# Optimization experiments

Hardware: AMD Instinct MI355X
Metric: run time of the kernel (lower is better)

Reference implementation:

```python
import jax, jax.numpy as jnp
import numpy as np

H = 64  # LSTM hidden size

def _lstm_layer(x, Wih, Whh, bih, bhh):
    # x: [B,T,I]; PyTorch gate order (i, f, g, o); zero initial state
    B, T, _ = x.shape
    pre = jnp.einsum('bti,gi->btg', x, Wih) + bih + bhh  # [B,T,4H]
    def step(carry, p):
        h, c = carry
        g = p + h @ Whh.T
        i, f, gg, o = jnp.split(g, 4, axis=-1)
        c = jax.nn.sigmoid(f) * c + jax.nn.sigmoid(i) * jnp.tanh(gg)
        h = jax.nn.sigmoid(o) * jnp.tanh(c)
        return (h, c), h
    h0 = jnp.zeros((B, H), x.dtype)
    c0 = jnp.zeros((B, H), x.dtype)
    _, hs = jax.lax.scan(step, (h0, c0), jnp.swapaxes(pre, 0, 1))
    return jnp.swapaxes(hs, 0, 1)  # [B,T,H]

def _lstm_params(key, in_dim):
    s = 1.0 / np.sqrt(H)
    k1, k2, k3, k4 = jax.random.split(key, 4)
    return (jax.random.uniform(k1, (4 * H, in_dim), jnp.float32, -s, s),
            jax.random.uniform(k2, (4 * H, H), jnp.float32, -s, s),
            jax.random.uniform(k3, (4 * H,), jnp.float32, -s, s),
            jax.random.uniform(k4, (4 * H,), jnp.float32, -s, s))

def setup_inputs() -> dict:
    key = jax.random.key(0)
    ks = jax.random.split(key, 9)
    B, T = 1024, 1024
    x = jax.random.normal(ks[0], (B, T, 3), jnp.float32)
    e1 = _lstm_params(ks[1], 3)
    e2 = _lstm_params(ks[2], H)
    d1 = _lstm_params(ks[3], 5)
    d2 = _lstm_params(ks[4], H)
    s = 1.0 / np.sqrt(H)
    enc_fc_W = jax.random.uniform(ks[5], (5, H), jnp.float32, -s, s)
    enc_fc_b = jax.random.uniform(ks[6], (5,), jnp.float32, -s, s)
    dec_fc_W = jax.random.uniform(ks[7], (3, H), jnp.float32, -s, s)
    dec_fc_b = jax.random.uniform(ks[8], (3,), jnp.float32, -s, s)
    return {
        'x': x,
        'e1_Wih': e1[0], 'e1_Whh': e1[1], 'e1_bih': e1[2], 'e1_bhh': e1[3],
        'e2_Wih': e2[0], 'e2_Whh': e2[1], 'e2_bih': e2[2], 'e2_bhh': e2[3],
        'enc_fc_W': enc_fc_W, 'enc_fc_b': enc_fc_b,
        'd1_Wih': d1[0], 'd1_Whh': d1[1], 'd1_bih': d1[2], 'd1_bhh': d1[3],
        'd2_Wih': d2[0], 'd2_Whh': d2[1], 'd2_bih': d2[2], 'd2_bhh': d2[3],
        'dec_fc_W': dec_fc_W, 'dec_fc_b': dec_fc_b,
    }

def reference(x,
              e1_Wih, e1_Whh, e1_bih, e1_bhh,
              e2_Wih, e2_Whh, e2_bih, e2_bhh,
              enc_fc_W, enc_fc_b,
              d1_Wih, d1_Whh, d1_bih, d1_bhh,
              d2_Wih, d2_Whh, d2_bih, d2_bhh,
              dec_fc_W, dec_fc_b):
    h = _lstm_layer(x, e1_Wih, e1_Whh, e1_bih, e1_bhh)
    h = _lstm_layer(h, e2_Wih, e2_Whh, e2_bih, e2_bhh)
    u = h[:, -1, :] @ enc_fc_W.T + enc_fc_b        # [B,5]
    u = u[:, None, :]                               # [B,1,5]
    d = _lstm_layer(u, d1_Wih, d1_Whh, d1_bih, d1_bhh)
    d = _lstm_layer(d, d2_Wih, d2_Whh, d2_bih, d2_bhh)
    tau = d[:, -1, :] @ dec_fc_W.T + dec_fc_b       # [B,3]
    return (u, tau)
```

## Files before the change

### kernel.cpp

```cpp
#include <hip/hip_runtime.h>
#include <stdint.h>

typedef _Float16 f16x8 __attribute__((ext_vector_type(8)));
typedef float f32x4 __attribute__((ext_vector_type(4)));

__device__ __forceinline__ float sigf(float x) {
    return __builtin_amdgcn_rcpf(1.0f + __expf(-x));
}
__device__ __forceinline__ float tanhf_fast(float x) {
    return 1.0f - 2.0f * __builtin_amdgcn_rcpf(1.0f + __expf(2.0f * x));
}
__device__ __forceinline__ uint32_t pk2f(float a, float b) {
    uint16_t ua = __builtin_bit_cast(uint16_t, (_Float16)a);
    uint16_t ub = __builtin_bit_cast(uint16_t, (_Float16)b);
    return (uint32_t)ua | ((uint32_t)ub << 16);
}

__global__ __launch_bounds__(512, 1)
void lstm_mfma16(const float* __restrict__ x,
                 const float* __restrict__ W1i, const float* __restrict__ W1h,
                 const float* __restrict__ b1i, const float* __restrict__ b1h,
                 const float* __restrict__ W2i, const float* __restrict__ W2h,
                 const float* __restrict__ b2i, const float* __restrict__ b2h,
                 const float* __restrict__ eW,  const float* __restrict__ eb,
                 const float* __restrict__ D1i, const float* __restrict__ D1bi,
                 const float* __restrict__ D1bh,
                 const float* __restrict__ D2i, const float* __restrict__ D2bi,
                 const float* __restrict__ D2bh,
                 const float* __restrict__ dW,  const float* __restrict__ db,
                 float* __restrict__ out)
{
    __shared__ __align__(16) _Float16 h1b[2][16][72];
    __shared__ __align__(16) _Float16 h2b[2][16][72];
    __shared__ __align__(16) _Float16 xs[2][16][16][8];
    __shared__ float uW[8][8];
    __shared__ float tlA[8][64];
    __shared__ float tlB[8][64];

    const int tid = threadIdx.x, blk = blockIdx.x;
    const int wid = tid >> 6, lane = tid & 63;
    const int rl = lane & 15, hi = lane >> 4;
    const bool isL1 = (wid < 4);
    const int w = isL1 ? wid : wid - 4;

    {
        uint32_t* z1 = (uint32_t*)&h1b[0][0][0];
        for (int i = tid; i < 1152; i += 512) z1[i] = 0u;
        uint32_t* z2 = (uint32_t*)&h2b[0][0][0];
        for (int i = tid; i < 1152; i += 512) z2[i] = 0u;
        uint32_t* z3 = (uint32_t*)&xs[0][0][0][0];
        for (int i = tid; i < 2048; i += 512) z3[i] = 0u;
    }

    f16x8 afr[4][4];
    #pragma unroll
    for (int g = 0; g < 4; ++g) {
        const int grow = g * 64 + w * 16 + rl;
        if (isL1) {
            #pragma unroll
            for (int s = 0; s < 2; ++s) {
                f16x8 v;
                #pragma unroll
                for (int i = 0; i < 8; ++i)
                    v[i] = (_Float16)W1h[grow * 64 + s * 32 + hi * 8 + i];
                afr[g][s] = v;
            }
            {
                f16x8 v;
                #pragma unroll
                for (int i = 0; i < 8; ++i) {
                    int kk = hi * 8 + i;
                    v[i] = (kk < 3) ? (_Float16)W1i[grow * 3 + kk] : (_Float16)0.0f;
                }
                afr[g][2] = v;
            }
            {
                f16x8 v;
                #pragma unroll
                for (int i = 0; i < 8; ++i) v[i] = (_Float16)0.0f;
                afr[g][3] = v;
            }
        } else {
            #pragma unroll
            for (int s = 0; s < 2; ++s) {
                f16x8 v;
                #pragma unroll
                for (int i = 0; i < 8; ++i)
                    v[i] = (_Float16)W2i[grow * 64 + s * 32 + hi * 8 + i];
                afr[g][s] = v;
            }
            #pragma unroll
            for (int s = 0; s < 2; ++s) {
                f16x8 v;
                #pragma unroll
                for (int i = 0; i < 8; ++i)
                    v[i] = (_Float16)W2h[grow * 64 + s * 32 + hi * 8 + i];
                afr[g][2 + s] = v;
            }
        }
    }

    f32x4 bias[4];
    #pragma unroll
    for (int g = 0; g < 4; ++g) {
        #pragma unroll
        for (int r = 0; r < 4; ++r) {
            int grow = g * 64 + w * 16 + hi * 4 + r;
            bias[g][r] = isL1 ? (b1i[grow] + b1h[grow]) : (b2i[grow] + b2h[grow]);
        }
    }

    float cst[4] = {0.0f, 0.0f, 0.0f, 0.0f};

    const int tt = tid >> 4, sA = tid & 15;
    const float* xsrc = x + (size_t)(blk * 16 + sA) * 3072;
    float xr0 = 0.f, xr1 = 0.f, xr2 = 0.f;

    __syncthreads();

    if (tid < 256) {
        const float* xp = xsrc + (size_t)tt * 3;
        uint2 pk;
        pk.x = pk2f(xp[0], xp[1]);
        pk.y = pk2f(xp[2], 0.0f);
        *(uint2*)&xs[0][tt][sA][0] = pk;
    }
    __syncthreads();

    #pragma unroll 1
    for (int t = 0; t <= 1024; ++t) {
        const int p = t & 1;
        const int cb = (t >> 4) & 1;

        if ((t & 15) == 0 && (t + 16) < 1024 && tid < 256) {
            const float* xp = xsrc + (size_t)(t + 16 + tt) * 3;
            xr0 = xp[0]; xr1 = xp[1]; xr2 = xp[2];
        }

        if (isL1 && t < 1024) {
            f32x4 a0 = bias[0], a1 = bias[1], a2 = bias[2], a3 = bias[3];
            #pragma unroll
            for (int s = 0; s < 2; ++s) {
                f16x8 bf = *(const f16x8*)&h1b[p][rl][s * 32 + hi * 8];
                a0 = __builtin_amdgcn_mfma_f32_16x16x32_f16(afr[0][s], bf, a0, 0, 0, 0);
                a1 = __builtin_amdgcn_mfma_f32_16x16x32_f16(afr[1][s], bf, a1, 0, 0, 0);
                a2 = __builtin_amdgcn_mfma_f32_16x16x32_f16(afr[2][s], bf, a2, 0, 0, 0);
                a3 = __builtin_amdgcn_mfma_f32_16x16x32_f16(afr[3][s], bf, a3, 0, 0, 0);
            }
            {
                f16x8 bf = {};
                if (hi == 0) bf = *(const f16x8*)&xs[cb][t & 15][rl][0];
                a0 = __builtin_amdgcn_mfma_f32_16x16x32_f16(afr[0][2], bf, a0, 0, 0, 0);
                a1 = __builtin_amdgcn_mfma_f32_16x16x32_f16(afr[1][2], bf, a1, 0, 0, 0);
                a2 = __builtin_amdgcn_mfma_f32_16x16x32_f16(afr[2][2], bf, a2, 0, 0, 0);
                a3 = __builtin_amdgcn_mfma_f32_16x16x32_f16(afr[3][2], bf, a3, 0, 0, 0);
            }
            uint16_t hu[4];
            #pragma unroll
            for (int r = 0; r < 4; ++r) {
                float pi = a0[r], pf = a1[r], pgg = a2[r], po = a3[r];
                cst[r] = sigf(pf) * cst[r] + sigf(pi) * tanhf_fast(pgg);
                float hn = sigf(po) * tanhf_fast(cst[r]);
                hu[r] = __builtin_bit_cast(uint16_t, (_Float16)hn);
            }
            uint2 pk;
            pk.x = (uint32_t)hu[0] | ((uint32_t)hu[1] << 16);
            pk.y = (uint32_t)hu[2] | ((uint32_t)hu[3] << 16);
            *(uint2*)&h1b[p ^ 1][rl][w * 16 + hi * 4] = pk;
        } else if (!isL1 && t >= 1) {
            f32x4 a0 = bias[0], a1 = bias[1], a2 = bias[2], a3 = bias[3];
            #pragma unroll
            for (int s = 0; s < 2; ++s) {
                f16x8 bf = *(const f16x8*)&h1b[p][rl][s * 32 + hi * 8];
                a0 = __builtin_amdgcn_mfma_f32_16x16x32_f16(afr[0][s], bf, a0, 0, 0, 0);
                a1 = __builtin_amdgcn_mfma_f32_16x16x32_f16(afr[1][s], bf, a1, 0, 0, 0);
                a2 = __builtin_amdgcn_mfma_f32_16x16x32_f16(afr[2][s], bf, a2, 0, 0, 0);
                a3 = __builtin_amdgcn_mfma_f32_16x16x32_f16(afr[3][s], bf, a3, 0, 0, 0);
            }
            #pragma unroll
            for (int s = 0; s < 2; ++s) {
                f16x8 bf = *(const f16x8*)&h2b[p][rl][s * 32 + hi * 8];
                a0 = __builtin_amdgcn_mfma_f32_16x16x32_f16(afr[0][2 + s], bf, a0, 0, 0, 0);
                a1 = __builtin_amdgcn_mfma_f32_16x16x32_f16(afr[1][2 + s], bf, a1, 0, 0, 0);
                a2 = __builtin_amdgcn_mfma_f32_16x16x32_f16(afr[2][2 + s], bf, a2, 0, 0, 0);
                a3 = __builtin_amdgcn_mfma_f32_16x16x32_f16(afr[3][2 + s], bf, a3, 0, 0, 0);
            }
            uint16_t hu[4];
            #pragma unroll
            for (int r = 0; r < 4; ++r) {
                float pi = a0[r], pf = a1[r], pgg = a2[r], po = a3[r];
                cst[r] = sigf(pf) * cst[r] + sigf(pi) * tanhf_fast(pgg);
                float hn = sigf(po) * tanhf_fast(cst[r]);
                hu[r] = __builtin_bit_cast(uint16_t, (_Float16)hn);
            }
            uint2 pk;
            pk.x = (uint32_t)hu[0] | ((uint32_t)hu[1] << 16);
            pk.y = (uint32_t)hu[2] | ((uint32_t)hu[3] << 16);
            *(uint2*)&h2b[p ^ 1][rl][w * 16 + hi * 4] = pk;
        }

        if ((t & 15) == 15 && (t + 1) < 1024 && tid < 256) {
            uint2 pk;
            pk.x = pk2f(xr0, xr1);
            pk.y = pk2f(xr2, 0.0f);
            *(uint2*)&xs[cb ^ 1][tt][sA][0] = pk;
        }
        __syncthreads();
    }

    #pragma unroll 1
    for (int ss = 0; ss < 2; ++ss) {
        const int s = wid * 2 + ss;
        const int S = blk * 16 + s;

        if (lane < 5) {
            float acc = eb[lane];
            for (int k = 0; k < 64; ++k)
                acc += eW[lane * 64 + k] * (float)h2b[1][s][k];
            uW[wid][lane] = acc;
            out[S * 5 + lane] = acc;
        }
        __syncthreads();

        {
            float u0 = uW[wid][0], u1 = uW[wid][1], u2 = uW[wid][2],
                  u3 = uW[wid][3], u4 = uW[wid][4];
            int ri = lane, rg = 128 + lane, ro = 192 + lane;
            float pi = D1bi[ri] + D1bh[ri];
            float pg = D1bi[rg] + D1bh[rg];
            float po = D1bi[ro] + D1bh[ro];
            pi += D1i[ri*5+0]*u0 + D1i[ri*5+1]*u1 + D1i[ri*5+2]*u2 + D1i[ri*5+3]*u3 + D1i[ri*5+4]*u4;
            pg += D1i[rg*5+0]*u0 + D1i[rg*5+1]*u1 + D1i[rg*5+2]*u2 + D1i[rg*5+3]*u3 + D1i[rg*5+4]*u4;
            po += D1i[ro*5+0]*u0 + D1i[ro*5+1]*u1 + D1i[ro*5+2]*u2 + D1i[ro*5+3]*u3 + D1i[ro*5+4]*u4;
            float cd = sigf(pi) * tanhf_fast(pg);
            float hd = sigf(po) * tanhf_fast(cd);
            tlA[wid][lane] = hd;
        }
        __syncthreads();

        {
            int ri = lane, rg = 128 + lane, ro = 192 + lane;
            float pi = D2bi[ri] + D2bh[ri];
            float pg = D2bi[rg] + D2bh[rg];
            float po = D2bi[ro] + D2bh[ro];
            for (int k = 0; k < 64; ++k) {
                float hk = tlA[wid][k];
                pi += D2i[ri * 64 + k] * hk;
                pg += D2i[rg * 64 + k] * hk;
                po += D2i[ro * 64 + k] * hk;
            }
            float cd = sigf(pi) * tanhf_fast(pg);
            float hd = sigf(po) * tanhf_fast(cd);
            tlB[wid][lane] = hd;
        }
        __syncthreads();

        if (lane < 3) {
            float acc = db[lane];
            for (int k = 0; k < 64; ++k) acc += dW[lane * 64 + k] * tlB[wid][k];
            out[5120 + S * 3 + lane] = acc;
        }
        __syncthreads();
    }
}

extern "C" void kernel_launch(void* const* d_in, const int* in_sizes, int n_in,
                              void* d_out, int out_size, void* d_ws, size_t ws_size,
                              hipStream_t stream) {
    (void)in_sizes; (void)n_in; (void)out_size; (void)d_ws; (void)ws_size;
    const float* x    = (const float*)d_in[0];
    const float* W1i  = (const float*)d_in[1];
    const float* W1h  = (const float*)d_in[2];
    const float* b1i  = (const float*)d_in[3];
    const float* b1h  = (const float*)d_in[4];
    const float* W2i  = (const float*)d_in[5];
    const float* W2h  = (const float*)d_in[6];
    const float* b2i  = (const float*)d_in[7];
    const float* b2h  = (const float*)d_in[8];
    const float* eW   = (const float*)d_in[9];
    const float* eb   = (const float*)d_in[10];
    const float* D1i  = (const float*)d_in[11];
    const float* D1bi = (const float*)d_in[13];
    const float* D1bh = (const float*)d_in[14];
    const float* D2i  = (const float*)d_in[15];
    const float* D2bi = (const float*)d_in[17];
    const float* D2bh = (const float*)d_in[18];
    const float* dW   = (const float*)d_in[19];
    const float* db   = (const float*)d_in[20];

    hipLaunchKernelGGL(lstm_mfma16, dim3(64), dim3(512), 0, stream,
                       x, W1i, W1h, b1i, b1h, W2i, W2h, b2i, b2h, eW, eb,
                       D1i, D1bi, D1bh, D2i, D2bi, D2bh, dW, db,
                       (float*)d_out);
}
```

Baseline: 984.0 us.

## Halve sequences per block to 8, doubling grid, and prescale gate weights by log2e

```diff
diff --git a/kernel.cpp b/kernel.cpp
--- a/kernel.cpp
+++ b/kernel.cpp
@@ -1,9 +1,18 @@
 #include <hip/hip_runtime.h>
 #include <stdint.h>
+#include <math.h>
 
 typedef _Float16 f16x8 __attribute__((ext_vector_type(8)));
 typedef float f32x4 __attribute__((ext_vector_type(4)));
 
+#define LOG2E 1.44269504088896340736f
+
+__device__ __forceinline__ float sigp(float p) {
+    return __builtin_amdgcn_rcpf(1.0f + exp2f(-p));
+}
+__device__ __forceinline__ float tanhg(float p) {
+    return 1.0f - 2.0f * __builtin_amdgcn_rcpf(1.0f + exp2f(p));
+}
 __device__ __forceinline__ float sigf(float x) {
     return __builtin_amdgcn_rcpf(1.0f + __expf(-x));
 }
@@ -17,18 +26,18 @@
 }
 
 __global__ __launch_bounds__(512, 1)
-void lstm_mfma16(const float* __restrict__ x,
-                 const float* __restrict__ W1i, const float* __restrict__ W1h,
-                 const float* __restrict__ b1i, const float* __restrict__ b1h,
-                 const float* __restrict__ W2i, const float* __restrict__ W2h,
-                 const float* __restrict__ b2i, const float* __restrict__ b2h,
-                 const float* __restrict__ eW,  const float* __restrict__ eb,
-                 const float* __restrict__ D1i, const float* __restrict__ D1bi,
-                 const float* __restrict__ D1bh,
-                 const float* __restrict__ D2i, const float* __restrict__ D2bi,
-                 const float* __restrict__ D2bh,
-                 const float* __restrict__ dW,  const float* __restrict__ db,
-                 float* __restrict__ out)
+void lstm_mfma8(const float* __restrict__ x,
+                const float* __restrict__ W1i, const float* __restrict__ W1h,
+                const float* __restrict__ b1i, const float* __restrict__ b1h,
+                const float* __restrict__ W2i, const float* __restrict__ W2h,
+                const float* __restrict__ b2i, const float* __restrict__ b2h,
+                const float* __restrict__ eW,  const float* __restrict__ eb,
+                const float* __restrict__ D1i, const float* __restrict__ D1bi,
+                const float* __restrict__ D1bh,
+                const float* __restrict__ D2i, const float* __restrict__ D2bi,
+                const float* __restrict__ D2bh,
+                const float* __restrict__ dW,  const float* __restrict__ db,
+                float* __restrict__ out)
 {
     __shared__ __align__(16) _Float16 h1b[2][16][72];
     __shared__ __align__(16) _Float16 h2b[2][16][72];
@@ -52,17 +61,20 @@
         for (int i = tid; i < 2048; i += 512) z3[i] = 0u;
     }
 
+    const float gsc[4] = {LOG2E, LOG2E, 2.0f * LOG2E, LOG2E};
+
     f16x8 afr[4][4];
     #pragma unroll
     for (int g = 0; g < 4; ++g) {
         const int grow = g * 64 + w * 16 + rl;
+        const float sc = gsc[g];
         if (isL1) {
             #pragma unroll
             for (int s = 0; s < 2; ++s) {
                 f16x8 v;
                 #pragma unroll
                 for (int i = 0; i < 8; ++i)
-                    v[i] = (_Float16)W1h[grow * 64 + s * 32 + hi * 8 + i];
+                    v[i] = (_Float16)(sc * W1h[grow * 64 + s * 32 + hi * 8 + i]);
                 afr[g][s] = v;
             }
             {
@@ -70,7 +82,7 @@
                 #pragma unroll
                 for (int i = 0; i < 8; ++i) {
                     int kk = hi * 8 + i;
-                    v[i] = (kk < 3) ? (_Float16)W1i[grow * 3 + kk] : (_Float16)0.0f;
+                    v[i] = (kk < 3) ? (_Float16)(sc * W1i[grow * 3 + kk]) : (_Float16)0.0f;
                 }
                 afr[g][2] = v;
             }
@@ -86,7 +98,7 @@
                 f16x8 v;
                 #pragma unroll
                 for (int i = 0; i < 8; ++i)
-                    v[i] = (_Float16)W2i[grow * 64 + s * 32 + hi * 8 + i];
+                    v[i] = (_Float16)(sc * W2i[grow * 64 + s * 32 + hi * 8 + i]);
                 afr[g][s] = v;
             }
             #pragma unroll
@@ -94,7 +106,7 @@
                 f16x8 v;
                 #pragma unroll
                 for (int i = 0; i < 8; ++i)
-                    v[i] = (_Float16)W2h[grow * 64 + s * 32 + hi * 8 + i];
+                    v[i] = (_Float16)(sc * W2h[grow * 64 + s * 32 + hi * 8 + i]);
                 afr[g][2 + s] = v;
             }
         }
@@ -106,19 +118,20 @@
         #pragma unroll
         for (int r = 0; r < 4; ++r) {
             int grow = g * 64 + w * 16 + hi * 4 + r;
-            bias[g][r] = isL1 ? (b1i[grow] + b1h[grow]) : (b2i[grow] + b2h[grow]);
+            bias[g][r] = gsc[g] * (isL1 ? (b1i[grow] + b1h[grow])
+                                        : (b2i[grow] + b2h[grow]));
         }
     }
 
     float cst[4] = {0.0f, 0.0f, 0.0f, 0.0f};
 
-    const int tt = tid >> 4, sA = tid & 15;
-    const float* xsrc = x + (size_t)(blk * 16 + sA) * 3072;
+    const int tt = tid >> 3, sA = tid & 7;
+    const float* xsrc = x + (size_t)(blk * 8 + sA) * 3072;
     float xr0 = 0.f, xr1 = 0.f, xr2 = 0.f;
 
     __syncthreads();
 
-    if (tid < 256) {
+    if (tid < 128) {
         const float* xp = xsrc + (size_t)tt * 3;
         uint2 pk;
         pk.x = pk2f(xp[0], xp[1]);
@@ -132,7 +145,7 @@
         const int p = t & 1;
         const int cb = (t >> 4) & 1;
 
-        if ((t & 15) == 0 && (t + 16) < 1024 && tid < 256) {
+        if ((t & 15) == 0 && (t + 16) < 1024 && tid < 128) {
             const float* xp = xsrc + (size_t)(t + 16 + tt) * 3;
             xr0 = xp[0]; xr1 = xp[1]; xr2 = xp[2];
         }
@@ -155,18 +168,20 @@
                 a2 = __builtin_amdgcn_mfma_f32_16x16x32_f16(afr[2][2], bf, a2, 0, 0, 0);
                 a3 = __builtin_amdgcn_mfma_f32_16x16x32_f16(afr[3][2], bf, a3, 0, 0, 0);
             }
-            uint16_t hu[4];
-            #pragma unroll
-            for (int r = 0; r < 4; ++r) {
-                float pi = a0[r], pf = a1[r], pgg = a2[r], po = a3[r];
-                cst[r] = sigf(pf) * cst[r] + sigf(pi) * tanhf_fast(pgg);
-                float hn = sigf(po) * tanhf_fast(cst[r]);
-                hu[r] = __builtin_bit_cast(uint16_t, (_Float16)hn);
-            }
-            uint2 pk;
-            pk.x = (uint32_t)hu[0] | ((uint32_t)hu[1] << 16);
-            pk.y = (uint32_t)hu[2] | ((uint32_t)hu[3] << 16);
-            *(uint2*)&h1b[p ^ 1][rl][w * 16 + hi * 4] = pk;
+            if (rl < 8) {
+                uint16_t hu[4];
+                #pragma unroll
+                for (int r = 0; r < 4; ++r) {
+                    float pi = a0[r], pf = a1[r], pgg = a2[r], po = a3[r];
+                    cst[r] = sigp(pf) * cst[r] + sigp(pi) * tanhg(pgg);
+                    float hn = sigp(po) * tanhg(2.0f * LOG2E * cst[r]);
+                    hu[r] = __builtin_bit_cast(uint16_t, (_Float16)hn);
+                }
+                uint2 pk;
+                pk.x = (uint32_t)hu[0] | ((uint32_t)hu[1] << 16);
+                pk.y = (uint32_t)hu[2] | ((uint32_t)hu[3] << 16);
+                *(uint2*)&h1b[p ^ 1][rl][w * 16 + hi * 4] = pk;
+            }
         } else if (!isL1 && t >= 1) {
             f32x4 a0 = bias[0], a1 = bias[1], a2 = bias[2], a3 = bias[3];
             #pragma unroll
@@ -185,21 +200,23 @@
                 a2 = __builtin_amdgcn_mfma_f32_16x16x32_f16(afr[2][2 + s], bf, a2, 0, 0, 0);
                 a3 = __builtin_amdgcn_mfma_f32_16x16x32_f16(afr[3][2 + s], bf, a3, 0, 0, 0);
             }
-            uint16_t hu[4];
-            #pragma unroll
-            for (int r = 0; r < 4; ++r) {
-                float pi = a0[r], pf = a1[r], pgg = a2[r], po = a3[r];
-                cst[r] = sigf(pf) * cst[r] + sigf(pi) * tanhf_fast(pgg);
-                float hn = sigf(po) * tanhf_fast(cst[r]);
-                hu[r] = __builtin_bit_cast(uint16_t, (_Float16)hn);
-            }
-            uint2 pk;
-            pk.x = (uint32_t)hu[0] | ((uint32_t)hu[1] << 16);
-            pk.y = (uint32_t)hu[2] | ((uint32_t)hu[3] << 16);
-            *(uint2*)&h2b[p ^ 1][rl][w * 16 + hi * 4] = pk;
-        }
-
-        if ((t & 15) == 15 && (t + 1) < 1024 && tid < 256) {
+            if (rl < 8) {
+                uint16_t hu[4];
+                #pragma unroll
+                for (int r = 0; r < 4; ++r) {
+                    float pi = a0[r], pf = a1[r], pgg = a2[r], po = a3[r];
+                    cst[r] = sigp(pf) * cst[r] + sigp(pi) * tanhg(pgg);
+                    float hn = sigp(po) * tanhg(2.0f * LOG2E * cst[r]);
+                    hu[r] = __builtin_bit_cast(uint16_t, (_Float16)hn);
+                }
+                uint2 pk;
+                pk.x = (uint32_t)hu[0] | ((uint32_t)hu[1] << 16);
+                pk.y = (uint32_t)hu[2] | ((uint32_t)hu[3] << 16);
+                *(uint2*)&h2b[p ^ 1][rl][w * 16 + hi * 4] = pk;
+            }
+        }
+
+        if ((t & 15) == 15 && (t + 1) < 1024 && tid < 128) {
             uint2 pk;
             pk.x = pk2f(xr0, xr1);
             pk.y = pk2f(xr2, 0.0f);
@@ -208,59 +225,55 @@
         __syncthreads();
     }
 
-    #pragma unroll 1
-    for (int ss = 0; ss < 2; ++ss) {
-        const int s = wid * 2 + ss;
-        const int S = blk * 16 + s;
-
-        if (lane < 5) {
-            float acc = eb[lane];
-            for (int k = 0; k < 64; ++k)
-                acc += eW[lane * 64 + k] * (float)h2b[1][s][k];
-            uW[wid][lane] = acc;
-            out[S * 5 + lane] = acc;
-        }
-        __syncthreads();
-
-        {
-            float u0 = uW[wid][0], u1 = uW[wid][1], u2 = uW[wid][2],
-                  u3 = uW[wid][3], u4 = uW[wid][4];
-            int ri = lane, rg = 128 + lane, ro = 192 + lane;
-            float pi = D1bi[ri] + D1bh[ri];
-            float pg = D1bi[rg] + D1bh[rg];
-            float po = D1bi[ro] + D1bh[ro];
-            pi += D1i[ri*5+0]*u0 + D1i[ri*5+1]*u1 + D1i[ri*5+2]*u2 + D1i[ri*5+3]*u3 + D1i[ri*5+4]*u4;
-            pg += D1i[rg*5+0]*u0 + D1i[rg*5+1]*u1 + D1i[rg*5+2]*u2 + D1i[rg*5+3]*u3 + D1i[rg*5+4]*u4;
-            po += D1i[ro*5+0]*u0 + D1i[ro*5+1]*u1 + D1i[ro*5+2]*u2 + D1i[ro*5+3]*u3 + D1i[ro*5+4]*u4;
-            float cd = sigf(pi) * tanhf_fast(pg);
-            float hd = sigf(po) * tanhf_fast(cd);
-            tlA[wid][lane] = hd;
-        }
-        __syncthreads();
-
-        {
-            int ri = lane, rg = 128 + lane, ro = 192 + lane;
-            float pi = D2bi[ri] + D2bh[ri];
-            float pg = D2bi[rg] + D2bh[rg];
-            float po = D2bi[ro] + D2bh[ro];
-            for (int k = 0; k < 64; ++k) {
-                float hk = tlA[wid][k];
-                pi += D2i[ri * 64 + k] * hk;
-                pg += D2i[rg * 64 + k] * hk;
-                po += D2i[ro * 64 + k] * hk;
-            }
-            float cd = sigf(pi) * tanhf_fast(pg);
-            float hd = sigf(po) * tanhf_fast(cd);
-            tlB[wid][lane] = hd;
-        }
-        __syncthreads();
-
-        if (lane < 3) {
-            float acc = db[lane];
-            for (int k = 0; k < 64; ++k) acc += dW[lane * 64 + k] * tlB[wid][k];
-            out[5120 + S * 3 + lane] = acc;
-        }
-        __syncthreads();
+    const int s = wid;
+    const int S = blk * 8 + s;
+
+    if (lane < 5) {
+        float acc = eb[lane];
+        for (int k = 0; k < 64; ++k)
+            acc += eW[lane * 64 + k] * (float)h2b[1][s][k];
+        uW[wid][lane] = acc;
+        out[S * 5 + lane] = acc;
+    }
+    __syncthreads();
+
+    {
+        float u0 = uW[wid][0], u1 = uW[wid][1], u2 = uW[wid][2],
+              u3 = uW[wid][3], u4 = uW[wid][4];
+        int ri = lane, rg = 128 + lane, ro = 192 + lane;
+        float pi = D1bi[ri] + D1bh[ri];
+        float pg = D1bi[rg] + D1bh[rg];
+        float po = D1bi[ro] + D1bh[ro];
+        pi += D1i[ri*5+0]*u0 + D1i[ri*5+1]*u1 + D1i[ri*5+2]*u2 + D1i[ri*5+3]*u3 + D1i[ri*5+4]*u4;
+        pg += D1i[rg*5+0]*u0 + D1i[rg*5+1]*u1 + D1i[rg*5+2]*u2 + D1i[rg*5+3]*u3 + D1i[rg*5+4]*u4;
+        po += D1i[ro*5+0]*u0 + D1i[ro*5+1]*u1 + D1i[ro*5+2]*u2 + D1i[ro*5+3]*u3 + D1i[ro*5+4]*u4;
+        float cd = sigf(pi) * tanhf_fast(pg);
+        float hd = sigf(po) * tanhf_fast(cd);
+        tlA[wid][lane] = hd;
+    }
+    __syncthreads();
+
+    {
+        int ri = lane, rg = 128 + lane, ro = 192 + lane;
+        float pi = D2bi[ri] + D2bh[ri];
+        float pg = D2bi[rg] + D2bh[rg];
+        float po = D2bi[ro] + D2bh[ro];
+        for (int k = 0; k < 64; ++k) {
+            float hk = tlA[wid][k];
+            pi += D2i[ri * 64 + k] * hk;
+            pg += D2i[rg * 64 + k] * hk;
+            po += D2i[ro * 64 + k] * hk;
+        }
+        float cd = sigf(pi) * tanhf_fast(pg);
+        float hd = sigf(po) * tanhf_fast(cd);
+        tlB[wid][lane] = hd;
+    }
+    __syncthreads();
+
+    if (lane < 3) {
+        float acc = db[lane];
+        for (int k = 0; k < 64; ++k) acc += dW[lane * 64 + k] * tlB[wid][k];
+        out[5120 + S * 3 + lane] = acc;
     }
 }
 
@@ -288,7 +301,7 @@
     const float* dW   = (const float*)d_in[19];
     const float* db   = (const float*)d_in[20];
 
-    hipLaunchKernelGGL(lstm_mfma16, dim3(64), dim3(512), 0, stream,
+    hipLaunchKernelGGL(lstm_mfma8, dim3(128), dim3(512), 0, stream,
                        x, W1i, W1h, b1i, b1h, W2i, W2h, b2i, b2h, eW, eb,
                        D1i, D1bi, D1bh, D2i, D2bi, D2bh, dW, db,
                        (float*)d_out);
```

Result: slower. 1.226 ms (+24.6%).
